# Optimization experiments

Measured on AMD Instinct MI355X. Metric: run time of the kernel, lower is better.

## Reference

```python
import jax, jax.numpy as jnp
import numpy as np

M_FACTORS = [8, 8, 8, 8]
N_FACTORS = [8, 8, 8, 8]
RANK = 8
E = 8
B = 8
SEQ = 512
M_IN = int(np.prod(M_FACTORS))   # 4096
N_OUT = int(np.prod(N_FACTORS))  # 4096


def setup_inputs() -> dict:
    key = jax.random.key(0)
    k1, k2, k3, k4, k5 = jax.random.split(key, 5)
    X = jax.random.normal(k1, (B, SEQ, M_IN), dtype=jnp.float32)
    gates = jax.random.uniform(k2, (B, E), dtype=jnp.float32)
    # TT cores: [E, r_i, factor, r_{i+1}]; boundary ranks are 1.
    core_first = jax.random.normal(k3, (E, 1, M_FACTORS[0], RANK), dtype=jnp.float32)
    cores_mid = jax.random.normal(k4, (6, E, RANK, 8, RANK), dtype=jnp.float32)
    core_last = jax.random.normal(k5, (E, RANK, N_FACTORS[-1], 1), dtype=jnp.float32)
    return {"X": X, "gates": gates, "core_first": core_first,
            "cores_mid": cores_mid, "core_last": core_last}


def _tt_forward(X, gates, core_first, cores_mid, core_last):
    b, s, _ = X.shape
    # View X as [B, 1, seq, m_k-1, ..., m_0] (m factors reversed), rank dim = 1.
    tt = X.reshape((b, s) + tuple(M_FACTORS[::-1]))[:, None]
    cores = [core_first] + [cores_mid[i] for i in range(cores_mid.shape[0])] + [core_last]
    num_m = len(M_FACTORS)
    # Input-factor contractions: 'b r ... m, b r m p -> b p ...'
    for i in range(num_m):
        merged = jnp.einsum('be,ermp->brmp', gates, cores[i])  # [B, r, m_f, p]
        tt = jnp.einsum('br...m,brmp->bp...', tt, merged)
    # Output-factor expansions: 'b r ..., b r n p -> b p ... n'
    for i in range(len(N_FACTORS)):
        merged = jnp.einsum('be,ernp->brnp', gates, cores[num_m + i])  # [B, r, n_f, p]
        tt = jnp.einsum('br...,brnp->bp...n', tt, merged)
    return tt.reshape(b, s, -1)  # [B, seq, prod(n_factors)]


def reference(X, gates, core_first, cores_mid, core_last):
    return _tt_forward(X, gates, core_first, cores_mid, core_last)
```

## Files before the change

kernel.cpp:

```cpp
#include <hip/hip_runtime.h>


#define MC_     32
#define MCHUNK_ 128

__global__ __launch_bounds__(256) void k_compose(
    const float* __restrict__ gates,
    const float* __restrict__ core_first,
    const float* __restrict__ cores_mid,
    const float* __restrict__ core_last,
    float* __restrict__ Kin,
    float* __restrict__ Kout)
{
  const int part = blockIdx.x;
  const int b    = blockIdx.y;
  const int t    = threadIdx.x;

  __shared__ float g[8];
  __shared__ float mg[3200];
  __shared__ __align__(16) float A2[512];
  __shared__ __align__(16) float A3[4096];
  __shared__ __align__(16) float C2[512];
  __shared__ __align__(16) float C3[4096];

  if (t < 8) g[t] = gates[b*8 + t];
  __syncthreads();

  for (int idx = t; idx < 3200; idx += 256) {
    float acc = 0.f;
    if (idx < 64) {
      #pragma unroll
      for (int e = 0; e < 8; ++e) acc += g[e] * core_first[e*64 + idx];
    } else if (idx < 3136) {
      const int i = (idx - 64) >> 9;
      const int w = (idx - 64) & 511;
      #pragma unroll
      for (int e = 0; e < 8; ++e) acc += g[e] * cores_mid[(i*8 + e)*512 + w];
    } else {
      const int w = idx - 3136;
      #pragma unroll
      for (int e = 0; e < 8; ++e) acc += g[e] * core_last[e*64 + w];
    }
    mg[idx] = acc;
  }
  __syncthreads();

  const float* mg0 = mg;
  const float* mg1 = mg + 64;
  const float* mg2 = mg + 64 + 512;
  const float* mg3 = mg + 64 + 1024;
  const float* mg4 = mg + 64 + 1536;
  const float* mg5 = mg + 64 + 2048;
  const float* mg6 = mg + 64 + 2560;
  const float* mg7 = mg + 3136;

  for (int idx = t; idx < 1024; idx += 256) {
    if (idx < 512) {
      const int mm = idx >> 3, p2 = idx & 7;
      const int m1 = mm >> 3, m0 = mm & 7;
      float acc = 0.f;
      #pragma unroll
      for (int p1 = 0; p1 < 8; ++p1)
        acc += mg0[m0*8 + p1] * mg1[p1*64 + m1*8 + p2];
      A2[idx] = acc;
    } else {
      const int id = idx - 512;
      const int p6 = id >> 6, n2 = (id >> 3) & 7, n3 = id & 7;
      float acc = 0.f;
      #pragma unroll
      for (int p7 = 0; p7 < 8; ++p7)
        acc += mg6[p6*64 + n2*8 + p7] * mg7[p7*8 + n3];
      C2[id] = acc;
    }
  }
  __syncthreads();

  for (int idx = t; idx < 8192; idx += 256) {
    if (idx < 4096) {
      const int rest = idx >> 3, p3 = idx & 7;
      const int m2 = rest >> 6, mm = rest & 63;
      float acc = 0.f;
      #pragma unroll
      for (int p2 = 0; p2 < 8; ++p2)
        acc += A2[mm*8 + p2] * mg2[p2*64 + m2*8 + p3];
      A3[idx] = acc;
    } else {
      const int id = idx - 4096;
      const int p5 = id >> 9, n1 = (id >> 6) & 7, nn = id & 63;
      float acc = 0.f;
      #pragma unroll
      for (int p6 = 0; p6 < 8; ++p6)
        acc += mg5[p5*64 + n1*8 + p6] * C2[p6*64 + nn];
      C3[id] = acc;
    }
  }
  __syncthreads();

  {
    float* kb = Kin + b*32768 + part*4096;
    #pragma unroll
    for (int rr = 0; rr < 2; ++rr) {
      const int r = t*2 + rr;
      #pragma unroll
      for (int p4 = 0; p4 < 8; ++p4) {
        float acc = 0.f;
        #pragma unroll
        for (int p3 = 0; p3 < 8; ++p3)
          acc += A3[r*8 + p3] * mg3[p3*64 + part*8 + p4];
        kb[r*8 + p4] = acc;
      }
    }
    float* ob = Kout + b*32768 + part*512;
    #pragma unroll
    for (int jj = 0; jj < 2; ++jj) {
      const int j = t*2 + jj;
      #pragma unroll
      for (int p4 = 0; p4 < 8; ++p4) {
        float acc = 0.f;
        #pragma unroll
        for (int p5 = 0; p5 < 8; ++p5)
          acc += mg4[p4*64 + part*8 + p5] * C3[p5*512 + j];
        ob[p4*4096 + j] = acc;
      }
    }
  }
}

__global__ __launch_bounds__(256) void k_vpart(
    const float* __restrict__ X,
    const float* __restrict__ Kin,
    float* __restrict__ Vpart)
{
  const int mc = blockIdx.x;
  const int sg = blockIdx.y;
  const int b  = blockIdx.z;
  const int t  = threadIdx.x;

  __shared__ __align__(16) float lk[MCHUNK_ * 8];
  ((float4*)lk)[t] = ((const float4*)(Kin + b*32768 + mc*(MCHUNK_*8)))[t];
  __syncthreads();

  const int s = sg*256 + t;
  const float4* xr = (const float4*)(X + (size_t)(b*512 + s)*4096 + mc*MCHUNK_);

  float acc[8];
  #pragma unroll
  for (int p = 0; p < 8; ++p) acc[p] = 0.f;

  #pragma unroll 8
  for (int j = 0; j < MCHUNK_/4; ++j) {
    const float4 x4 = xr[j];
    const float* kp = &lk[j*32];
    #pragma unroll
    for (int p = 0; p < 8; ++p) acc[p] += x4.x * kp[p];
    #pragma unroll
    for (int p = 0; p < 8; ++p) acc[p] += x4.y * kp[8 + p];
    #pragma unroll
    for (int p = 0; p < 8; ++p) acc[p] += x4.z * kp[16 + p];
    #pragma unroll
    for (int p = 0; p < 8; ++p) acc[p] += x4.w * kp[24 + p];
  }

  float* vp = Vpart + ((size_t)(b*MC_ + mc)*512 + s)*8;
  *(float4*)(vp)     = make_float4(acc[0], acc[1], acc[2], acc[3]);
  *(float4*)(vp + 4) = make_float4(acc[4], acc[5], acc[6], acc[7]);
}

__global__ __launch_bounds__(256) void k_out(
    const float* __restrict__ Vpart,
    const float* __restrict__ Kout,
    float* __restrict__ Out)
{
  const int nc = blockIdx.x;
  const int sg = blockIdx.y;
  const int b  = blockIdx.z;
  const int t  = threadIdx.x;

  __shared__ __align__(16) float vs[32*8];

  {
    const float* vp = Vpart + ((size_t)b*MC_*512 + sg*32)*8 + t;
    float a = 0.f;
    #pragma unroll 8
    for (int mc = 0; mc < MC_; ++mc) a += vp[(size_t)mc*512*8];
    vs[t] = a;
  }

  float4 kr[8];
  {
    const float* kb = Kout + b*32768 + nc*1024 + t*4;
    #pragma unroll
    for (int p = 0; p < 8; ++p) kr[p] = *(const float4*)(kb + p*4096);
  }
  __syncthreads();

  float* ob = Out + (size_t)(b*512 + sg*32)*4096 + nc*1024 + t*4;
  for (int s = 0; s < 32; ++s) {
    const float* vv = &vs[s*8];
    float o0 = 0.f, o1 = 0.f, o2 = 0.f, o3 = 0.f;
    #pragma unroll
    for (int p = 0; p < 8; ++p) {
      const float v = vv[p];
      o0 += v * kr[p].x; o1 += v * kr[p].y; o2 += v * kr[p].z; o3 += v * kr[p].w;
    }
    *(float4*)(ob + (size_t)s*4096) = make_float4(o0, o1, o2, o3);
  }
}

extern "C" void kernel_launch(void* const* d_in, const int* in_sizes, int n_in,
                              void* d_out, int out_size, void* d_ws, size_t ws_size,
                              hipStream_t stream) {
  const float* X     = (const float*)d_in[0];
  const float* gates = (const float*)d_in[1];
  const float* cf    = (const float*)d_in[2];
  const float* cm    = (const float*)d_in[3];
  const float* cl    = (const float*)d_in[4];
  float* out = (float*)d_out;

  float* ws    = (float*)d_ws;
  float* Kin   = ws;
  float* Kout  = ws + 262144;
  float* Vpart = ws + 524288;

  k_compose<<<dim3(8, 8),        256, 0, stream>>>(gates, cf, cm, cl, Kin, Kout);
  k_vpart <<<dim3(MC_, 2, 8),    256, 0, stream>>>(X, Kin, Vpart);
  k_out   <<<dim3(4, 16, 8),     256, 0, stream>>>(Vpart, Kout, out);
}
```

Baseline: 140.3 us.

## Restructure X-by-Kin projection to stage coalesced X tiles in shared memory

The reduction of X against the composed input core is rewritten. Each block now loads a 16-row by 512-column X tile into padded LDS with coalesced float4 loads, plus a transposed Kin chunk. Threads compute dot products split across two halves, which are then reduced in LDS. The M dimension now uses 8 chunks instead of 32, which also shrinks the partial-sum buffer that k_out has to reduce. The old layout gave each thread its own strided X row, so global loads were uncoalesced. The cost is about 50 KB of LDS per block, which limits occupancy, and an extra synchronization plus reduction step.

```diff
diff --git a/kernel.cpp b/kernel.cpp
--- a/kernel.cpp
+++ b/kernel.cpp
@@ -1,8 +1,7 @@
 #include <hip/hip_runtime.h>
 
 
-#define MC_     32
-#define MCHUNK_ 128
+#define MC_ 8
 
 __global__ __launch_bounds__(256) void k_compose(
     const float* __restrict__ gates,
@@ -126,44 +125,71 @@
   }
 }
 
+#define XPAD 516
+
 __global__ __launch_bounds__(256) void k_vpart(
     const float* __restrict__ X,
     const float* __restrict__ Kin,
     float* __restrict__ Vpart)
 {
-  const int mc = blockIdx.x;
-  const int sg = blockIdx.y;
-  const int b  = blockIdx.z;
-  const int t  = threadIdx.x;
-
-  __shared__ __align__(16) float lk[MCHUNK_ * 8];
-  ((float4*)lk)[t] = ((const float4*)(Kin + b*32768 + mc*(MCHUNK_*8)))[t];
-  __syncthreads();
-
-  const int s = sg*256 + t;
-  const float4* xr = (const float4*)(X + (size_t)(b*512 + s)*4096 + mc*MCHUNK_);
-
-  float acc[8];
-  #pragma unroll
-  for (int p = 0; p < 8; ++p) acc[p] = 0.f;
-
-  #pragma unroll 8
-  for (int j = 0; j < MCHUNK_/4; ++j) {
-    const float4 x4 = xr[j];
-    const float* kp = &lk[j*32];
-    #pragma unroll
-    for (int p = 0; p < 8; ++p) acc[p] += x4.x * kp[p];
-    #pragma unroll
-    for (int p = 0; p < 8; ++p) acc[p] += x4.y * kp[8 + p];
-    #pragma unroll
-    for (int p = 0; p < 8; ++p) acc[p] += x4.z * kp[16 + p];
-    #pragma unroll
-    for (int p = 0; p < 8; ++p) acc[p] += x4.w * kp[24 + p];
-  }
-
-  float* vp = Vpart + ((size_t)(b*MC_ + mc)*512 + s)*8;
-  *(float4*)(vp)     = make_float4(acc[0], acc[1], acc[2], acc[3]);
-  *(float4*)(vp + 4) = make_float4(acc[4], acc[5], acc[6], acc[7]);
+  const int stile = blockIdx.x;
+  const int mc    = blockIdx.y;
+  const int b     = blockIdx.z;
+  const int t     = threadIdx.x;
+
+  __shared__ __align__(16) float xs[16 * XPAD];
+  __shared__ __align__(16) float lkT[8 * XPAD];
+  __shared__ float vred[2 * 16 * 8];
+
+  {
+    const float* xbase = X + ((size_t)(b*512 + stile*16) * 4096) + mc*512;
+    #pragma unroll
+    for (int i = 0; i < 8; ++i) {
+      const int idx = t + i*256;
+      const int r = idx >> 7;
+      const int c = idx & 127;
+      const float4 v = ((const float4*)(xbase + (size_t)r*4096))[c];
+      *(float4*)&xs[r*XPAD + c*4] = v;
+    }
+  }
+  {
+    const float4* kb = (const float4*)(Kin + b*32768 + mc*4096);
+    #pragma unroll
+    for (int i = 0; i < 4; ++i) {
+      const int idx = t + i*256;
+      const int m  = idx >> 1;
+      const int ph = (idx & 1) * 4;
+      const float4 v = kb[idx];
+      lkT[(ph+0)*XPAD + m] = v.x;
+      lkT[(ph+1)*XPAD + m] = v.y;
+      lkT[(ph+2)*XPAD + m] = v.z;
+      lkT[(ph+3)*XPAD + m] = v.w;
+    }
+  }
+  __syncthreads();
+
+  {
+    const int h  = t >> 7;
+    const int sp = t & 127;
+    const int sl = sp >> 3;
+    const int p  = sp & 7;
+    const float* xrow = &xs[sl*XPAD + h*256];
+    const float* krow = &lkT[p*XPAD + h*256];
+    float acc = 0.f;
+    #pragma unroll 8
+    for (int j = 0; j < 64; ++j) {
+      const float4 a = *(const float4*)(xrow + j*4);
+      const float4 k = *(const float4*)(krow + j*4);
+      acc += a.x*k.x + a.y*k.y + a.z*k.z + a.w*k.w;
+    }
+    vred[t] = acc;
+  }
+  __syncthreads();
+
+  if (t < 128) {
+    const float v = vred[t] + vred[128 + t];
+    Vpart[((size_t)(b*MC_ + mc)*512 + stile*16)*8 + t] = v;
+  }
 }
 
 __global__ __launch_bounds__(256) void k_out(
@@ -181,7 +207,7 @@
   {
     const float* vp = Vpart + ((size_t)b*MC_*512 + sg*32)*8 + t;
     float a = 0.f;
-    #pragma unroll 8
+    #pragma unroll
     for (int mc = 0; mc < MC_; ++mc) a += vp[(size_t)mc*512*8];
     vs[t] = a;
   }
@@ -222,7 +248,7 @@
   float* Kout  = ws + 262144;
   float* Vpart = ws + 524288;
 
-  k_compose<<<dim3(8, 8),        256, 0, stream>>>(gates, cf, cm, cl, Kin, Kout);
-  k_vpart <<<dim3(MC_, 2, 8),    256, 0, stream>>>(X, Kin, Vpart);
-  k_out   <<<dim3(4, 16, 8),     256, 0, stream>>>(Vpart, Kout, out);
-}
+  k_compose<<<dim3(8, 8),          256, 0, stream>>>(gates, cf, cm, cl, Kin, Kout);
+  k_vpart <<<dim3(32, MC_, 8),     256, 0, stream>>>(X, Kin, Vpart);
+  k_out   <<<dim3(4, 16, 8),       256, 0, stream>>>(Vpart, Kout, out);
+}
```

Measured after the change: 136.1 us. 1.03x faster.

## Store Kin in bf16 and restructure k_vpart for coalesced X reads with shuffle reduction

Applied to the files above, without the earlier changes.

Kin, the composed input-side TT matrix, is now written in bf16 and read directly from global memory as packed uint4 instead of being staged in LDS. k_vpart is remapped so 16 rows per wave each have four lanes striding across the m chunk, which makes X loads more coalesced. Partial sums are combined with cross-lane shuffles, and the number of m chunks drops to 16. The bf16 rounding of Kin adds numerical error, and the different mapping changes the occupancy and cache behaviour of the kernel that streams X.

```diff
diff --git a/kernel.cpp b/kernel.cpp
--- a/kernel.cpp
+++ b/kernel.cpp
@@ -1,15 +1,15 @@
 #include <hip/hip_runtime.h>
-
-
-#define MC_     32
-#define MCHUNK_ 128
+#include <hip/hip_bf16.h>
+
+
+#define MC_ 16
 
 __global__ __launch_bounds__(256) void k_compose(
     const float* __restrict__ gates,
     const float* __restrict__ core_first,
     const float* __restrict__ cores_mid,
     const float* __restrict__ core_last,
-    float* __restrict__ Kin,
+    __hip_bfloat16* __restrict__ Kinb,
     float* __restrict__ Kout)
 {
   const int part = blockIdx.x;
@@ -97,7 +97,7 @@
   __syncthreads();
 
   {
-    float* kb = Kin + b*32768 + part*4096;
+    __hip_bfloat16* kb = Kinb + ((size_t)b*4096 + part*512)*8;
     #pragma unroll
     for (int rr = 0; rr < 2; ++rr) {
       const int r = t*2 + rr;
@@ -107,7 +107,7 @@
         #pragma unroll
         for (int p3 = 0; p3 < 8; ++p3)
           acc += A3[r*8 + p3] * mg3[p3*64 + part*8 + p4];
-        kb[r*8 + p4] = acc;
+        kb[r*8 + p4] = __float2bfloat16(acc);
       }
     }
     float* ob = Kout + b*32768 + part*512;
@@ -126,44 +126,62 @@
   }
 }
 
+__device__ __forceinline__ float bfhi(unsigned u) {
+  return __uint_as_float(u & 0xffff0000u);
+}
+__device__ __forceinline__ float bflo(unsigned u) {
+  return __uint_as_float(u << 16);
+}
+
 __global__ __launch_bounds__(256) void k_vpart(
     const float* __restrict__ X,
-    const float* __restrict__ Kin,
+    const uint4* __restrict__ Kinb,
     float* __restrict__ Vpart)
 {
-  const int mc = blockIdx.x;
-  const int sg = blockIdx.y;
+  const int sg = blockIdx.x;
+  const int mc = blockIdx.y;
   const int b  = blockIdx.z;
   const int t  = threadIdx.x;
 
-  __shared__ __align__(16) float lk[MCHUNK_ * 8];
-  ((float4*)lk)[t] = ((const float4*)(Kin + b*32768 + mc*(MCHUNK_*8)))[t];
-  __syncthreads();
-
-  const int s = sg*256 + t;
-  const float4* xr = (const float4*)(X + (size_t)(b*512 + s)*4096 + mc*MCHUNK_);
+  const int w = t >> 6;
+  const int l = t & 63;
+  const int r = l & 15;
+  const int q = l >> 4;
+
+  const int row = sg*64 + w*16 + r;
+  const float* xr = X + ((size_t)(b*512 + row))*4096 + mc*256 + q*4;
+  const uint4* kr = Kinb + (size_t)b*4096 + mc*256 + q*4;
 
   float acc[8];
   #pragma unroll
   for (int p = 0; p < 8; ++p) acc[p] = 0.f;
 
-  #pragma unroll 8
-  for (int j = 0; j < MCHUNK_/4; ++j) {
-    const float4 x4 = xr[j];
-    const float* kp = &lk[j*32];
-    #pragma unroll
-    for (int p = 0; p < 8; ++p) acc[p] += x4.x * kp[p];
-    #pragma unroll
-    for (int p = 0; p < 8; ++p) acc[p] += x4.y * kp[8 + p];
-    #pragma unroll
-    for (int p = 0; p < 8; ++p) acc[p] += x4.z * kp[16 + p];
-    #pragma unroll
-    for (int p = 0; p < 8; ++p) acc[p] += x4.w * kp[24 + p];
-  }
-
-  float* vp = Vpart + ((size_t)(b*MC_ + mc)*512 + s)*8;
-  *(float4*)(vp)     = make_float4(acc[0], acc[1], acc[2], acc[3]);
-  *(float4*)(vp + 4) = make_float4(acc[4], acc[5], acc[6], acc[7]);
+  #pragma unroll 4
+  for (int j = 0; j < 16; ++j) {
+    const float4 x4 = *(const float4*)(xr + j*16);
+    const float xv[4] = {x4.x, x4.y, x4.z, x4.w};
+    #pragma unroll
+    for (int i = 0; i < 4; ++i) {
+      const uint4 k8 = kr[j*16 + i];
+      const float xi = xv[i];
+      acc[0] += xi * bflo(k8.x);  acc[1] += xi * bfhi(k8.x);
+      acc[2] += xi * bflo(k8.y);  acc[3] += xi * bfhi(k8.y);
+      acc[4] += xi * bflo(k8.z);  acc[5] += xi * bfhi(k8.z);
+      acc[6] += xi * bflo(k8.w);  acc[7] += xi * bfhi(k8.w);
+    }
+  }
+
+  #pragma unroll
+  for (int p = 0; p < 8; ++p) {
+    acc[p] += __shfl_xor(acc[p], 16, 64);
+    acc[p] += __shfl_xor(acc[p], 32, 64);
+  }
+
+  if (l < 16) {
+    float* vp = Vpart + ((size_t)((b*MC_ + mc)*512) + row)*8;
+    *(float4*)(vp)     = make_float4(acc[0], acc[1], acc[2], acc[3]);
+    *(float4*)(vp + 4) = make_float4(acc[4], acc[5], acc[6], acc[7]);
+  }
 }
 
 __global__ __launch_bounds__(256) void k_out(
@@ -181,7 +199,7 @@
   {
     const float* vp = Vpart + ((size_t)b*MC_*512 + sg*32)*8 + t;
     float a = 0.f;
-    #pragma unroll 8
+    #pragma unroll
     for (int mc = 0; mc < MC_; ++mc) a += vp[(size_t)mc*512*8];
     vs[t] = a;
   }
@@ -217,12 +235,12 @@
   const float* cl    = (const float*)d_in[4];
   float* out = (float*)d_out;
 
-  float* ws    = (float*)d_ws;
-  float* Kin   = ws;
-  float* Kout  = ws + 262144;
-  float* Vpart = ws + 524288;
-
-  k_compose<<<dim3(8, 8),        256, 0, stream>>>(gates, cf, cm, cl, Kin, Kout);
-  k_vpart <<<dim3(MC_, 2, 8),    256, 0, stream>>>(X, Kin, Vpart);
+  float* ws = (float*)d_ws;
+  float*          Kout  = ws;
+  float*          Vpart = ws + 262144;
+  __hip_bfloat16* Kinb  = (__hip_bfloat16*)(ws + 262144 + 524288);
+
+  k_compose<<<dim3(8, 8),        256, 0, stream>>>(gates, cf, cm, cl, Kinb, Kout);
+  k_vpart <<<dim3(8, MC_, 8),    256, 0, stream>>>(X, (const uint4*)Kinb, Vpart);
   k_out   <<<dim3(4, 16, 8),     256, 0, stream>>>(Vpart, Kout, out);
 }
```

Measured after the change: 145.4 us. +3.6%, slower.
